# Kernel tuning notes

Hardware: AMD Instinct MI355X
Metric: run time of the kernel (lower is better)

The kernel has to match this reference:

```python
import jax, jax.numpy as jnp
import numpy as np


def setup_inputs() -> dict:
    key = jax.random.key(0)
    k1, k2 = jax.random.split(key)
    B, N, M = 2, 8192, 8192
    source_point_cloud = jax.random.normal(k1, (B, N, 3), dtype=jnp.float32)
    target_point_cloud = jax.random.normal(k2, (B, M, 3), dtype=jnp.float32)
    return {"source_point_cloud": source_point_cloud,
            "target_point_cloud": target_point_cloud}


def reference(source_point_cloud, target_point_cloud):
    # source: [B, N, 3], target: [B, M, 3]
    s, t = source_point_cloud, target_point_cloud
    # Brute-force exact 1-NN (replaces per-batch CPU cKDTree query).
    # ||s - t||^2 = ||s||^2 + ||t||^2 - 2 s.t ; argmin unaffected by const terms per row,
    # but keep ||t||^2 since it varies over the argmin axis.
    s2 = jnp.sum(s * s, axis=-1)                       # [B, N]
    t2 = jnp.sum(t * t, axis=-1)                       # [B, M]
    dots = jnp.einsum('bnd,bmd->bnm', s, t)            # [B, N, M]
    d2 = t2[:, None, :] - 2.0 * dots                   # [B, N, M] (drop s2: row-constant)
    idx = jnp.argmin(d2, axis=-1)                      # [B, N] nearest target index
    target_points = jnp.take_along_axis(t, idx[..., None], axis=1)  # [B, N, 3]
    # MSELoss (mean over all elements) per batch, then mean over batch.
    per_batch = jnp.mean((s - target_points) ** 2, axis=(1, 2))     # [B]
    return jnp.mean(per_batch)
```

## Files before the change

### kernel.cpp

```cpp
#include <hip/hip_runtime.h>

#define BLOCK 256
#define SPT 4
#define MAX_CHUNK_M 512

__global__ __launch_bounds__(BLOCK) void nn_partial_kernel(
    const float* __restrict__ src, const float* __restrict__ tgt,
    float* __restrict__ partial, int N, int M, int SB, int C, int chunkM, int ST)
{
    __shared__ float4 tpts[MAX_CHUNK_M];

    const int c    = blockIdx.x % C;
    const int tmp  = blockIdx.x / C;
    const int sblk = tmp % SB;
    const int b    = tmp / SB;
    const int tid  = threadIdx.x;

    const int mbase = c * chunkM;
    const float* tb = tgt + (size_t)b * M * 3;
    for (int j = tid; j < chunkM; j += BLOCK) {
        int mi = mbase + j;
        float tx = 0.f, ty = 0.f, tz = 0.f;
        float t2 = 1e30f;
        if (mi < M) {
            tx = tb[(size_t)mi * 3 + 0];
            ty = tb[(size_t)mi * 3 + 1];
            tz = tb[(size_t)mi * 3 + 2];
            t2 = fmaf(tx, tx, fmaf(ty, ty, tz * tz));
        }
        tpts[j] = make_float4(tx, ty, tz, t2);
    }
    __syncthreads();

    const int sbase = sblk * (BLOCK * SPT);
    const float* sbp = src + (size_t)b * N * 3;
    float nsx[SPT], nsy[SPT], nsz[SPT], mind[SPT];
#pragma unroll
    for (int s = 0; s < SPT; ++s) {
        int si = sbase + tid + s * BLOCK;
        float x = 0.f, y = 0.f, z = 0.f;
        if (si < N) {
            x = sbp[(size_t)si * 3 + 0];
            y = sbp[(size_t)si * 3 + 1];
            z = sbp[(size_t)si * 3 + 2];
        }
        nsx[s] = -2.f * x;
        nsy[s] = -2.f * y;
        nsz[s] = -2.f * z;
        mind[s] = 1e30f;
    }

#pragma unroll 4
    for (int m = 0; m < chunkM; ++m) {
        float4 tp = tpts[m];
#pragma unroll
        for (int s = 0; s < SPT; ++s) {
            float d = fmaf(nsx[s], tp.x, tp.w);
            d = fmaf(nsy[s], tp.y, d);
            d = fmaf(nsz[s], tp.z, d);
            mind[s] = fminf(mind[s], d);
        }
    }

#pragma unroll
    for (int s = 0; s < SPT; ++s) {
        int si = sbase + tid + s * BLOCK;
        if (si < N) {
            partial[(size_t)c * ST + (size_t)b * N + si] = mind[s];
        }
    }
}

__global__ __launch_bounds__(BLOCK) void nn_reduce_kernel(
    const float* __restrict__ src, const float* __restrict__ partial,
    float* __restrict__ out, int ST, int C, float scale)
{
    const int i = blockIdx.x * BLOCK + threadIdx.x;
    float v = 0.f;
    if (i < ST) {
        float sx = src[(size_t)i * 3 + 0];
        float sy = src[(size_t)i * 3 + 1];
        float sz = src[(size_t)i * 3 + 2];
        float mind = 1e30f;
        for (int c = 0; c < C; ++c) {
            mind = fminf(mind, partial[(size_t)c * ST + i]);
        }
        v = fmaf(sx, sx, fmaf(sy, sy, sz * sz)) + mind;
    }

#pragma unroll
    for (int off = 32; off > 0; off >>= 1) {
        v += __shfl_xor(v, off, 64);
    }

    __shared__ float wsum[BLOCK / 64];
    const int lane = threadIdx.x & 63;
    const int wav  = threadIdx.x >> 6;
    if (lane == 0) wsum[wav] = v;
    __syncthreads();
    if (threadIdx.x == 0) {
        float s = 0.f;
#pragma unroll
        for (int w = 0; w < BLOCK / 64; ++w) s += wsum[w];
        atomicAdd(out, s * scale);
    }
}

extern "C" void kernel_launch(void* const* d_in, const int* in_sizes, int n_in,
                              void* d_out, int out_size, void* d_ws, size_t ws_size,
                              hipStream_t stream) {
    const float* src = (const float*)d_in[0];
    const float* tgt = (const float*)d_in[1];
    float* out = (float*)d_out;

    const int B = 2;
    const int N = in_sizes[0] / (B * 3);
    const int M = in_sizes[1] / (B * 3);
    const int ST = B * N;

    int C = 32;
    while (C > 1 && (size_t)C * ST * sizeof(float) > ws_size) C >>= 1;
    int chunkM = (M + C - 1) / C;
    while (chunkM > MAX_CHUNK_M) { C <<= 1; chunkM = (M + C - 1) / C; }

    const int SB = (N + BLOCK * SPT - 1) / (BLOCK * SPT);
    float* partial = (float*)d_ws;

    hipMemsetAsync(d_out, 0, sizeof(float), stream);

    dim3 grid1(B * SB * C);
    nn_partial_kernel<<<grid1, BLOCK, 0, stream>>>(src, tgt, partial,
                                                   N, M, SB, C, chunkM, ST);

    dim3 grid2((ST + BLOCK - 1) / BLOCK);
    nn_reduce_kernel<<<grid2, BLOCK, 0, stream>>>(src, partial, out,
                                                  ST, C, 1.0f / (3.0f * N * B));
}
```

Before: 81.12 us.

## Fuse NN search and reduction into one kernel with in-block target slicing

Replaces the two-kernel scheme (per-chunk partial minima written to workspace, then a reduce kernel) with a single kernel. Each block handles 16 source points, split into two groups of 8, and its 128 lanes per group stride across all targets in tiles of 1024. Minima are combined with wave shuffles and shared memory, then atomically accumulated. This removes the partial-buffer traffic and the second launch, but every block reloads the full target set and does more per-point reduction work, and the many blocks (1024) each do an atomicAdd.

```diff
diff --git a/kernel.cpp b/kernel.cpp
--- a/kernel.cpp
+++ b/kernel.cpp
@@ -1,108 +1,100 @@
 #include <hip/hip_runtime.h>
 
-#define BLOCK 256
-#define SPT 4
-#define MAX_CHUNK_M 512
+#define BLOCK  256
+#define SPT    8
+#define SPB    16
+#define NSLICE 128
+#define CH     1024
 
-__global__ __launch_bounds__(BLOCK) void nn_partial_kernel(
+__global__ __launch_bounds__(BLOCK) void chamfer_min_kernel(
     const float* __restrict__ src, const float* __restrict__ tgt,
-    float* __restrict__ partial, int N, int M, int SB, int C, int chunkM, int ST)
+    float* __restrict__ out, int N, int M, int total_src, float scale)
 {
-    __shared__ float4 tpts[MAX_CHUNK_M];
+    __shared__ float4 tpts[CH];
+    __shared__ float red[4][SPT];
 
-    const int c    = blockIdx.x % C;
-    const int tmp  = blockIdx.x / C;
-    const int sblk = tmp % SB;
-    const int b    = tmp / SB;
-    const int tid  = threadIdx.x;
+    const int tid = threadIdx.x;
+    const int g   = tid & (NSLICE - 1);
+    const int sg  = tid >> 7;
 
-    const int mbase = c * chunkM;
+    const int sbase = blockIdx.x * SPB + sg * SPT;
+    const int b = (sbase < total_src) ? (sbase / N) : 0;
+    const float* sb = src + (size_t)b * N * 3;
     const float* tb = tgt + (size_t)b * M * 3;
-    for (int j = tid; j < chunkM; j += BLOCK) {
-        int mi = mbase + j;
-        float tx = 0.f, ty = 0.f, tz = 0.f;
-        float t2 = 1e30f;
-        if (mi < M) {
-            tx = tb[(size_t)mi * 3 + 0];
-            ty = tb[(size_t)mi * 3 + 1];
-            tz = tb[(size_t)mi * 3 + 2];
-            t2 = fmaf(tx, tx, fmaf(ty, ty, tz * tz));
+
+    float nsx[SPT], nsy[SPT], nsz[SPT], s2[SPT], mind[SPT];
+    int vmask = 0;
+#pragma unroll
+    for (int u = 0; u < SPT; ++u) {
+        int gsi = sbase + u;
+        int si  = gsi - b * N;
+        bool ok = (gsi < total_src) && (si >= 0) && (si < N);
+        if (ok) vmask |= (1 << u);
+        float x = 0.f, y = 0.f, z = 0.f;
+        if (ok) {
+            x = sb[(size_t)si * 3 + 0];
+            y = sb[(size_t)si * 3 + 1];
+            z = sb[(size_t)si * 3 + 2];
         }
-        tpts[j] = make_float4(tx, ty, tz, t2);
+        nsx[u] = -2.f * x;
+        nsy[u] = -2.f * y;
+        nsz[u] = -2.f * z;
+        s2[u]  = fmaf(x, x, fmaf(y, y, z * z));
+        mind[u] = 1e30f;
+    }
+
+    for (int m0 = 0; m0 < M; m0 += CH) {
+        for (int j = tid; j < CH; j += BLOCK) {
+            int mi = m0 + j;
+            float tx = 0.f, ty = 0.f, tz = 0.f, t2 = 1e30f;
+            if (mi < M) {
+                tx = tb[(size_t)mi * 3 + 0];
+                ty = tb[(size_t)mi * 3 + 1];
+                tz = tb[(size_t)mi * 3 + 2];
+                t2 = fmaf(tx, tx, fmaf(ty, ty, tz * tz));
+            }
+            tpts[j] = make_float4(tx, ty, tz, t2);
+        }
+        __syncthreads();
+
+#pragma unroll
+        for (int k = 0; k < CH / NSLICE; ++k) {
+            float4 tp = tpts[k * NSLICE + g];
+#pragma unroll
+            for (int u = 0; u < SPT; ++u) {
+                float d = fmaf(nsx[u], tp.x,
+                          fmaf(nsy[u], tp.y,
+                          fmaf(nsz[u], tp.z, tp.w)));
+                mind[u] = fminf(mind[u], d);
+            }
+        }
+        __syncthreads();
+    }
+
+#pragma unroll
+    for (int u = 0; u < SPT; ++u) {
+#pragma unroll
+        for (int off = 1; off < 64; off <<= 1) {
+            mind[u] = fminf(mind[u], __shfl_xor(mind[u], off, 64));
+        }
+    }
+
+    const int lane = tid & 63;
+    const int w    = tid >> 6;
+    if (lane == 0) {
+#pragma unroll
+        for (int u = 0; u < SPT; ++u) red[w][u] = mind[u];
     }
     __syncthreads();
 
-    const int sbase = sblk * (BLOCK * SPT);
-    const float* sbp = src + (size_t)b * N * 3;
-    float nsx[SPT], nsy[SPT], nsz[SPT], mind[SPT];
+    if (lane == 0 && (w == 0 || w == 2)) {
+        float ssum = 0.f;
 #pragma unroll
-    for (int s = 0; s < SPT; ++s) {
-        int si = sbase + tid + s * BLOCK;
-        float x = 0.f, y = 0.f, z = 0.f;
-        if (si < N) {
-            x = sbp[(size_t)si * 3 + 0];
-            y = sbp[(size_t)si * 3 + 1];
-            z = sbp[(size_t)si * 3 + 2];
+        for (int u = 0; u < SPT; ++u) {
+            float mv = fminf(red[w][u], red[w + 1][u]);
+            if (vmask & (1 << u)) ssum += s2[u] + mv;
         }
-        nsx[s] = -2.f * x;
-        nsy[s] = -2.f * y;
-        nsz[s] = -2.f * z;
-        mind[s] = 1e30f;
-    }
-
-#pragma unroll 4
-    for (int m = 0; m < chunkM; ++m) {
-        float4 tp = tpts[m];
-#pragma unroll
-        for (int s = 0; s < SPT; ++s) {
-            float d = fmaf(nsx[s], tp.x, tp.w);
-            d = fmaf(nsy[s], tp.y, d);
-            d = fmaf(nsz[s], tp.z, d);
-            mind[s] = fminf(mind[s], d);
-        }
-    }
-
-#pragma unroll
-    for (int s = 0; s < SPT; ++s) {
-        int si = sbase + tid + s * BLOCK;
-        if (si < N) {
-            partial[(size_t)c * ST + (size_t)b * N + si] = mind[s];
-        }
-    }
-}
-
-__global__ __launch_bounds__(BLOCK) void nn_reduce_kernel(
-    const float* __restrict__ src, const float* __restrict__ partial,
-    float* __restrict__ out, int ST, int C, float scale)
-{
-    const int i = blockIdx.x * BLOCK + threadIdx.x;
-    float v = 0.f;
-    if (i < ST) {
-        float sx = src[(size_t)i * 3 + 0];
-        float sy = src[(size_t)i * 3 + 1];
-        float sz = src[(size_t)i * 3 + 2];
-        float mind = 1e30f;
-        for (int c = 0; c < C; ++c) {
-            mind = fminf(mind, partial[(size_t)c * ST + i]);
-        }
-        v = fmaf(sx, sx, fmaf(sy, sy, sz * sz)) + mind;
-    }
-
-#pragma unroll
-    for (int off = 32; off > 0; off >>= 1) {
-        v += __shfl_xor(v, off, 64);
-    }
-
-    __shared__ float wsum[BLOCK / 64];
-    const int lane = threadIdx.x & 63;
-    const int wav  = threadIdx.x >> 6;
-    if (lane == 0) wsum[wav] = v;
-    __syncthreads();
-    if (threadIdx.x == 0) {
-        float s = 0.f;
-#pragma unroll
-        for (int w = 0; w < BLOCK / 64; ++w) s += wsum[w];
-        atomicAdd(out, s * scale);
+        atomicAdd(out, ssum * scale);
     }
 }
 
@@ -116,23 +108,11 @@
     const int B = 2;
     const int N = in_sizes[0] / (B * 3);
     const int M = in_sizes[1] / (B * 3);
-    const int ST = B * N;
-
-    int C = 32;
-    while (C > 1 && (size_t)C * ST * sizeof(float) > ws_size) C >>= 1;
-    int chunkM = (M + C - 1) / C;
-    while (chunkM > MAX_CHUNK_M) { C <<= 1; chunkM = (M + C - 1) / C; }
-
-    const int SB = (N + BLOCK * SPT - 1) / (BLOCK * SPT);
-    float* partial = (float*)d_ws;
+    const int total_src = B * N;
 
     hipMemsetAsync(d_out, 0, sizeof(float), stream);
 
-    dim3 grid1(B * SB * C);
-    nn_partial_kernel<<<grid1, BLOCK, 0, stream>>>(src, tgt, partial,
-                                                   N, M, SB, C, chunkM, ST);
-
-    dim3 grid2((ST + BLOCK - 1) / BLOCK);
-    nn_reduce_kernel<<<grid2, BLOCK, 0, stream>>>(src, partial, out,
-                                                  ST, C, 1.0f / (3.0f * N * B));
+    const int grid = (total_src + SPB - 1) / SPB;
+    chamfer_min_kernel<<<grid, BLOCK, 0, stream>>>(
+        src, tgt, out, N, M, total_src, 1.0f / (3.0f * (float)N * (float)B));
 }
```

Result: slower. 98.28 us (+21.2%).
